# Optimization experiments

Hardware: AMD Instinct MI355X
Metric: run time of the kernel (lower is better)

Reference implementation:

```python
import jax, jax.numpy as jnp
import numpy as np

NU, NI, E, NNZ, NLAYERS, TOPK = 2560, 3584, 64, 200000, 2, 5
N = NU + NI
DQK = 4 * E  # Linear(dim, 4*dim)


def setup_inputs() -> dict:
    key = jax.random.key(0)
    ks = jax.random.split(key, 14)
    s = 1.0 / np.sqrt(E)
    return {
        "user_emb": jax.random.normal(ks[0], (NU, E), jnp.float32) * s,
        "item_emb": jax.random.normal(ks[1], (NI, E), jnp.float32) * s,
        "norm_rows": jax.random.randint(ks[2], (NNZ,), 0, N, jnp.int32),
        "norm_cols": jax.random.randint(ks[3], (NNZ,), 0, N, jnp.int32),
        "norm_vals": jax.random.uniform(ks[4], (NNZ,), jnp.float32) / 32.0,
        "adj_rows": jax.random.randint(ks[5], (NNZ,), 0, N, jnp.int32),
        "adj_cols": jax.random.randint(ks[6], (NNZ,), 0, N, jnp.int32),
        "adj_vals": jnp.ones((NNZ,), jnp.float32),
        "Wq": jax.random.normal(ks[7], (DQK, E), jnp.float32) * s,
        "bq": jnp.zeros((DQK,), jnp.float32),
        "Wk": jax.random.normal(ks[8], (DQK, E), jnp.float32) * s,
        "bk": jnp.zeros((DQK,), jnp.float32),
        "Wv": jax.random.normal(ks[9], (DQK, E), jnp.float32) * s,
        "bv": jnp.zeros((DQK,), jnp.float32),
    }


def reference(user_emb, item_emb, norm_rows, norm_cols, norm_vals,
              adj_rows, adj_cols, adj_vals, Wq, bq, Wk, bk, Wv, bv):
    # densified sparse adjacencies (duplicates accumulated, as COO spmm would)
    A_norm = jnp.zeros((N, N), jnp.float32).at[norm_rows, norm_cols].add(norm_vals)
    A = jnp.zeros((N, N), jnp.float32).at[adj_rows, adj_cols].add(adj_vals)

    ego = jnp.concatenate([user_emb, item_emb], axis=0)  # [N, E]
    layers = []
    att_out = None
    for _ in range(NLAYERS):
        layers.append(ego)
        # GNN propagation: sparse.mm(norm_adj, ego)
        ego = A_norm @ ego  # [N, E]
        # dense similarity + sparse-blended similarity
        sim = ego @ ego.T                      # [N, N]
        sim = sim + 0.5 * (A @ sim)            # [N, N]
        # top-K neighbor selection + gather
        _, idx = jax.lax.top_k(sim, TOPK)      # [N, K]
        sample = ego[idx]                      # [N, K, E]
        # SampleAttention: Linear(dim, 4*dim) Q/K/V, scaled dot-product over K neighbors
        q = ego @ Wq.T + bq                    # [N, 4E]
        kk = sample @ Wk.T + bk                # [N, K, 4E]
        vv = sample @ Wv.T + bv                # [N, K, 4E]
        scores = jnp.einsum('nd,nkd->nk', q, kk) / jnp.sqrt(jnp.float32(DQK))
        att = jax.nn.softmax(scores, axis=-1)
        att_out = jnp.einsum('nk,nkd->nd', att, vv)  # [N, 4E]
    mean_emb = jnp.mean(jnp.stack(layers, axis=1), axis=1)  # [N, E]
    return mean_emb[:NU], mean_emb[NU:], att_out
```

## Files before the change

### kernel.cpp

```cpp
#include <hip/hip_runtime.h>
#include <math.h>

#define NUSER 2560
#define NITEM 3584
#define NN    6144
#define EDIM  64
#define NNZ   200000
#define DQK   256
#define KTOP  5
#define SPLITS 16
#define TPS    3
#define CK     4
#define ELLW   96
#define TPB   256
#define QKV_BLOCKS 576
#define TOPK_BLOCKS (96 * SPLITS)
#define BSTR  72

typedef __attribute__((ext_vector_type(8))) short bf16x8;
typedef __attribute__((ext_vector_type(4))) float f32x4;

__device__ __forceinline__ unsigned short f2bf(float f) {
    unsigned int b = __float_as_uint(f);
    unsigned int r = (b + 0x7FFFu + ((b >> 16) & 1u)) >> 16;
    return (unsigned short)r;
}
__device__ __forceinline__ int pack2(float a, float b) {
    return (int)f2bf(a) | ((int)f2bf(b) << 16);
}
__device__ __forceinline__ void ell_unpack(long long v, int* col, float* w) {
    *col = (int)(v & 0xffffffffLL);
    *w   = __int_as_float((int)(v >> 32));
}
__device__ __forceinline__ unsigned umax(unsigned a, unsigned b) { return a > b ? a : b; }
__device__ __forceinline__ unsigned umin(unsigned a, unsigned b) { return a < b ? a : b; }

__global__ void build_kernel(const int* __restrict__ nr, const int* __restrict__ nc,
                             const float* __restrict__ nv,
                             const int* __restrict__ ar, const int* __restrict__ ac,
                             int* __restrict__ cnt_n, int* __restrict__ cnt_a,
                             long long* __restrict__ cv_n, int* __restrict__ cv_a) {
    int g = blockIdx.x * TPB + threadIdx.x;
    if (g < NNZ) {
        int r = __builtin_nontemporal_load(&nr[g]);
        int c = __builtin_nontemporal_load(&nc[g]);
        float v = __builtin_nontemporal_load(&nv[g]);
        int slot = atomicAdd(&cnt_n[r], 1);
        long long pk = (unsigned int)c | ((long long)(unsigned int)__float_as_int(v) << 32);
        __builtin_nontemporal_store(pk, &cv_n[r * ELLW + slot]);
    } else if (g < 2 * NNZ) {
        int h = g - NNZ;
        int r = __builtin_nontemporal_load(&ar[h]);
        int c = __builtin_nontemporal_load(&ac[h]);
        int slot = atomicAdd(&cnt_a[r], 1);
        __builtin_nontemporal_store(c, &cv_a[r * ELLW + slot]);
    }
}

__global__ __launch_bounds__(TPB) void spmm_ell_emb_kernel(
        const int* __restrict__ cnt, const long long* __restrict__ cv,
        const float* __restrict__ user, const float* __restrict__ item,
        float* __restrict__ dst) {
    int r = blockIdx.x * 4 + (threadIdx.x >> 6);
    int lane = threadIdx.x & 63;
    int s = r * ELLW, e = s + cnt[r];
    float a[8];
#pragma unroll
    for (int u = 0; u < 8; ++u) a[u] = 0.f;
    int j = s, n8 = s + ((e - s) & ~7);
    for (; j < n8; j += 8) {
        int col[8]; float w[8];
#pragma unroll
        for (int u = 0; u < 8; ++u) ell_unpack(__builtin_nontemporal_load(&cv[j + u]), &col[u], &w[u]);
#pragma unroll
        for (int u = 0; u < 8; ++u) {
            float x = (col[u] < NUSER) ? user[col[u] * EDIM + lane]
                                       : item[(col[u] - NUSER) * EDIM + lane];
            a[u] = fmaf(w[u], x, a[u]);
        }
    }
    for (; j < e; ++j) {
        int col; float w;
        ell_unpack(__builtin_nontemporal_load(&cv[j]), &col, &w);
        float x = (col < NUSER) ? user[col * EDIM + lane] : item[(col - NUSER) * EDIM + lane];
        a[0] = fmaf(w, x, a[0]);
    }
    dst[r * EDIM + lane] = ((a[0] + a[1]) + (a[2] + a[3])) + ((a[4] + a[5]) + (a[6] + a[7]));
}

__global__ __launch_bounds__(TPB) void spmm_ell_kernel(
        const int* __restrict__ cnt, const long long* __restrict__ cv,
        const float* __restrict__ src, float* __restrict__ dst,
        unsigned short* __restrict__ dsth) {
    int r = blockIdx.x * 4 + (threadIdx.x >> 6);
    int lane = threadIdx.x & 63;
    int s = r * ELLW, e = s + cnt[r];
    float a[8];
#pragma unroll
    for (int u = 0; u < 8; ++u) a[u] = 0.f;
    int j = s, n8 = s + ((e - s) & ~7);
    for (; j < n8; j += 8) {
        int col[8]; float w[8];
#pragma unroll
        for (int u = 0; u < 8; ++u) ell_unpack(__builtin_nontemporal_load(&cv[j + u]), &col[u], &w[u]);
#pragma unroll
        for (int u = 0; u < 8; ++u)
            a[u] = fmaf(w[u], src[col[u] * EDIM + lane], a[u]);
    }
    for (; j < e; ++j) {
        int col; float w;
        ell_unpack(__builtin_nontemporal_load(&cv[j]), &col, &w);
        a[0] = fmaf(w, src[col * EDIM + lane], a[0]);
    }
    float res = ((a[0] + a[1]) + (a[2] + a[3])) + ((a[4] + a[5]) + (a[6] + a[7]));
    dst[r * EDIM + lane]  = res;
    dsth[r * EDIM + lane] = f2bf(res);
}

__global__ __launch_bounds__(TPB) void qm_mean_kernel(
        const int* __restrict__ cnt, const int* __restrict__ cv,
        const float* __restrict__ ego2, const float* __restrict__ ego1,
        const float* __restrict__ user, const float* __restrict__ item,
        float* __restrict__ Qm, float* __restrict__ outmean) {
    int r = blockIdx.x * 4 + (threadIdx.x >> 6);
    int lane = threadIdx.x & 63;
    int s = r * ELLW, e = s + cnt[r];
    float a[8];
#pragma unroll
    for (int u = 0; u < 8; ++u) a[u] = 0.f;
    int j = s, n8 = s + ((e - s) & ~7);
    for (; j < n8; j += 8) {
        int col[8];
#pragma unroll
        for (int u = 0; u < 8; ++u) col[u] = __builtin_nontemporal_load(&cv[j + u]);
#pragma unroll
        for (int u = 0; u < 8; ++u)
            a[u] += ego2[col[u] * EDIM + lane];
    }
    for (; j < e; ++j) {
        int col = __builtin_nontemporal_load(&cv[j]);
        a[0] += ego2[col * EDIM + lane];
    }
    float acc = ((a[0] + a[1]) + (a[2] + a[3])) + ((a[4] + a[5]) + (a[6] + a[7]));
    int o = r * EDIM + lane;
    Qm[o] = ego2[o] + 0.5f * acc;
    float e0v = (r < NUSER) ? user[o] : item[o - NUSER * EDIM];
    outmean[o] = 0.5f * (e0v + ego1[o]);
}

__global__ __launch_bounds__(TPB) void qkv_gemm_kernel(
        const float* __restrict__ ego2,
        const float* __restrict__ Wq, const float* __restrict__ bq,
        const float* __restrict__ Wk, const float* __restrict__ bk,
        const float* __restrict__ Wv, const float* __restrict__ bv,
        float* __restrict__ Qa, float* __restrict__ Ka, float* __restrict__ Va) {
    __shared__ __align__(16) float smem[12288];
    int t = threadIdx.x;
    int tx = t & 15, ty = t >> 4;
    int id = blockIdx.x;
    int bz = id / 192, rem = id % 192, by = rem / 96, bx = rem % 96;
    const float* W; const float* b; float* out;
    if (bz == 0)      { W = Wq; b = bq; out = Qa; }
    else if (bz == 1) { W = Wk; b = bk; out = Ka; }
    else              { W = Wv; b = bv; out = Va; }
    float* As = smem;
    float* Bs = smem + 4096;
    int r0 = bx * 64, d0 = by * 128;
    {
        int r = t & 63, eb = (t >> 6) * 16;
#pragma unroll
        for (int rep = 0; rep < 4; ++rep) {
            int e0 = eb + rep * 4;
            float4 v = *(const float4*)&ego2[(r0 + r) * EDIM + e0];
            As[(e0 + 0) * 64 + r] = v.x; As[(e0 + 1) * 64 + r] = v.y;
            As[(e0 + 2) * 64 + r] = v.z; As[(e0 + 3) * 64 + r] = v.w;
        }
    }
    {
        int d = t & 127, eb = (t >> 7) * 32;
#pragma unroll
        for (int rep = 0; rep < 8; ++rep) {
            int e0 = eb + rep * 4;
            float4 v = *(const float4*)&W[(d0 + d) * EDIM + e0];
            Bs[(e0 + 0) * 128 + d] = v.x; Bs[(e0 + 1) * 128 + d] = v.y;
            Bs[(e0 + 2) * 128 + d] = v.z; Bs[(e0 + 3) * 128 + d] = v.w;
        }
    }
    __syncthreads();
    float acc[4][8];
#pragma unroll
    for (int i = 0; i < 4; ++i)
#pragma unroll
        for (int j = 0; j < 8; ++j) acc[i][j] = 0.f;
#pragma unroll 4
    for (int e = 0; e < 64; ++e) {
        float4 a  = *(const float4*)&As[e * 64 + ty * 4];
        float4 b0 = *(const float4*)&Bs[e * 128 + tx * 4];
        float4 b1 = *(const float4*)&Bs[e * 128 + 64 + tx * 4];
        float ar[4] = {a.x, a.y, a.z, a.w};
#pragma unroll
        for (int i = 0; i < 4; ++i) {
            acc[i][0] = fmaf(ar[i], b0.x, acc[i][0]);
            acc[i][1] = fmaf(ar[i], b0.y, acc[i][1]);
            acc[i][2] = fmaf(ar[i], b0.z, acc[i][2]);
            acc[i][3] = fmaf(ar[i], b0.w, acc[i][3]);
            acc[i][4] = fmaf(ar[i], b1.x, acc[i][4]);
            acc[i][5] = fmaf(ar[i], b1.y, acc[i][5]);
            acc[i][6] = fmaf(ar[i], b1.z, acc[i][6]);
            acc[i][7] = fmaf(ar[i], b1.w, acc[i][7]);
        }
    }
    float4 bias0 = *(const float4*)&b[d0 + tx * 4];
    float4 bias1 = *(const float4*)&b[d0 + 64 + tx * 4];
#pragma unroll
    for (int i = 0; i < 4; ++i) {
        int r = r0 + ty * 4 + i;
        float4 o0 = make_float4(acc[i][0] + bias0.x, acc[i][1] + bias0.y,
                                acc[i][2] + bias0.z, acc[i][3] + bias0.w);
        float4 o1 = make_float4(acc[i][4] + bias1.x, acc[i][5] + bias1.y,
                                acc[i][6] + bias1.z, acc[i][7] + bias1.w);
        *(float4*)&out[r * DQK + d0 + tx * 4] = o0;
        *(float4*)&out[r * DQK + d0 + 64 + tx * 4] = o1;
    }
}

__global__ __launch_bounds__(TPB) void topk_kernel(
        const unsigned short* __restrict__ eg2h,
        const float* __restrict__ Qm,
        int* __restrict__ pidx) {
    __shared__ __align__(16) short smem[13312];
    int t = threadIdx.x;
    int id = blockIdx.x;
    int rb = id % 96, sp = id / 96;
    int r0 = rb * 64;
    int w = t >> 6, lane = t & 63, lq = lane >> 4, lc = lane & 15;

    short* Ah = smem;
    short* Bh = Ah + 64 * EDIM;

    {
        int row = t >> 2, seg = t & 3;
        const float4* src = (const float4*)&Qm[(size_t)(r0 + row) * EDIM + seg * 16];
        float4 f0 = src[0], f1 = src[1], f2 = src[2], f3 = src[3];
        int4 p0, p1;
        p0.x = pack2(f0.x, f0.y); p0.y = pack2(f0.z, f0.w);
        p0.z = pack2(f1.x, f1.y); p0.w = pack2(f1.z, f1.w);
        p1.x = pack2(f2.x, f2.y); p1.y = pack2(f2.z, f2.w);
        p1.z = pack2(f3.x, f3.y); p1.w = pack2(f3.z, f3.w);
        *(int4*)&Ah[row * EDIM + seg * 16] = p0;
        *(int4*)&Ah[row * EDIM + seg * 16 + 8] = p1;
    }

    int4 pr[4];
    {
        int c0 = (sp * TPS) * 128;
#pragma unroll
        for (int rep = 0; rep < 4; ++rep) {
            int v = t + 256 * rep;
            pr[rep] = *(const int4*)&eg2h[(size_t)(c0 + (v >> 3)) * EDIM + (v & 7) * 8];
        }
    }

    unsigned t3[4][3];
#pragma unroll
    for (int i = 0; i < 4; ++i)
#pragma unroll
        for (int k = 0; k < 3; ++k) t3[i][k] = 0u;

    const unsigned KMASK = 0xFFFFFFC0u;
    bf16x8 af0, af1;
    for (int tile = 0; tile < TPS; ++tile) {
        __syncthreads();
#pragma unroll
        for (int rep = 0; rep < 4; ++rep) {
            int v = t + 256 * rep;
            *(int4*)&Bh[(v >> 3) * BSTR + (v & 7) * 8] = pr[rep];
        }
        if (tile + 1 < TPS) {
            int c1 = (sp * TPS + tile + 1) * 128;
#pragma unroll
            for (int rep = 0; rep < 4; ++rep) {
                int v = t + 256 * rep;
                pr[rep] = *(const int4*)&eg2h[(size_t)(c1 + (v >> 3)) * EDIM + (v & 7) * 8];
            }
        }
        __syncthreads();
        if (tile == 0) {
            af0 = *(const bf16x8*)&Ah[(w * 16 + lc) * EDIM + lq * 8];
            af1 = *(const bf16x8*)&Ah[(w * 16 + lc) * EDIM + 32 + lq * 8];
        }

        int tb = tile * 8;
#pragma unroll
        for (int ch = 0; ch < 8; ++ch) {
            bf16x8 b0 = *(const bf16x8*)&Bh[(ch * 16 + lc) * BSTR + lq * 8];
            bf16x8 b1 = *(const bf16x8*)&Bh[(ch * 16 + lc) * BSTR + 32 + lq * 8];
            f32x4 acc = {16.f, 16.f, 16.f, 16.f};
            acc = __builtin_amdgcn_mfma_f32_16x16x32_bf16(af0, b0, acc, 0, 0, 0);
            acc = __builtin_amdgcn_mfma_f32_16x16x32_bf16(af1, b1, acc, 0, 0, 0);
            unsigned lid = (unsigned)(tb + ch);
#pragma unroll
            for (int reg = 0; reg < 4; ++reg) {
                unsigned key = (__float_as_uint(acc[reg]) & KMASK) | lid;
                unsigned v0 = t3[reg][0], v1 = t3[reg][1], v2 = t3[reg][2];
                t3[reg][0] = umax(v0, key);
                t3[reg][1] = umax(v1, umin(v0, key));
                t3[reg][2] = umax(v2, umin(v1, key));
            }
        }
    }

    int sb128 = sp * (TPS * 128);
    unsigned lc2 = (unsigned)(lc << 2);
#pragma unroll
    for (int i = 0; i < 4; ++i) {
        int row = r0 + w * 16 + lq * 4 + i;
        int base = (row * SPLITS + sp) * CK;
        unsigned a0 = t3[i][0], a1 = t3[i][1], a2 = t3[i][2];
#pragma unroll
        for (int k = 0; k < CK; ++k) {
            unsigned vk = (a0 & KMASK) | lc2;
            unsigned bvv = vk;
#pragma unroll
            for (int off = 1; off < 16; off <<= 1)
                bvv = umax(bvv, (unsigned)__shfl_xor((int)bvv, off, 64));
            if (vk == bvv) {
                unsigned lid = a0 & 63u;
                pidx[base + k] = sb128 + (int)((lid >> 3) << 7) + (int)((lid & 7) << 4) + lc;
                a0 = a1; a1 = a2; a2 = 0u;
            }
        }
    }
}

__global__ __launch_bounds__(TPB) void attn_kernel(
        const float* __restrict__ Qm, const float* __restrict__ ego2,
        const float* __restrict__ Qa, const float* __restrict__ Ka, const float* __restrict__ Va,
        const int* __restrict__ pidx, float* __restrict__ out) {
    __shared__ float sb[4][64];
    int wv = threadIdx.x >> 6, lane = threadIdx.x & 63;
    int r = blockIdx.x * 4 + wv;
    int ci0 = pidx[r * (SPLITS * CK) + lane];
    int part = lane & 3;

    const float4* qmp = (const float4*)(Qm + (size_t)r * EDIM + part * 16);
    float4 q0 = qmp[0], q1 = qmp[1], q2 = qmp[2], q3 = qmp[3];

#pragma unroll
    for (int p = 0; p < 4; ++p) {
        int j = p * 16 + (lane >> 2);
        int c = __shfl(ci0, j, 64);
        const float4* ep = (const float4*)(ego2 + (size_t)c * EDIM + part * 16);
        float4 e0 = ep[0], e1 = ep[1], e2 = ep[2], e3 = ep[3];
        float s = 0.f;
        s = fmaf(q0.x, e0.x, s); s = fmaf(q0.y, e0.y, s); s = fmaf(q0.z, e0.z, s); s = fmaf(q0.w, e0.w, s);
        s = fmaf(q1.x, e1.x, s); s = fmaf(q1.y, e1.y, s); s = fmaf(q1.z, e1.z, s); s = fmaf(q1.w, e1.w, s);
        s = fmaf(q2.x, e2.x, s); s = fmaf(q2.y, e2.y, s); s = fmaf(q2.z, e2.z, s); s = fmaf(q2.w, e2.w, s);
        s = fmaf(q3.x, e3.x, s); s = fmaf(q3.y, e3.y, s); s = fmaf(q3.z, e3.z, s); s = fmaf(q3.w, e3.w, s);
        s += __shfl_xor(s, 1, 64);
        s += __shfl_xor(s, 2, 64);
        if (part == 0) sb[wv][j] = s;
    }
    float sv = sb[wv][lane];

    float prevv = INFINITY; int previ = -1;
    int cI[KTOP];
#pragma unroll
    for (int k = 0; k < KTOP; ++k) {
        bool adm = (sv < prevv) || (sv == prevv && ci0 > previ);
        float bv = adm ? sv : -INFINITY;
        int   bi = adm ? ci0 : 0x7fffffff;
#pragma unroll
        for (int off = 1; off < 64; off <<= 1) {
            float ov = __shfl_xor(bv, off, 64);
            int   oi = __shfl_xor(bi, off, 64);
            if (ov > bv || (ov == bv && oi < bi)) { bv = ov; bi = oi; }
        }
        cI[k] = bi; prevv = bv; previ = bi;
    }

    float4 q = *(const float4*)&Qa[r * DQK + lane * 4];
    float sc[KTOP];
#pragma unroll
    for (int k = 0; k < KTOP; ++k) {
        float4 kk = *(const float4*)&Ka[cI[k] * DQK + lane * 4];
        float p = q.x * kk.x + q.y * kk.y + q.z * kk.z + q.w * kk.w;
#pragma unroll
        for (int off = 32; off; off >>= 1) p += __shfl_xor(p, off, 64);
        sc[k] = p * 0.0625f;
    }
    float m = sc[0];
#pragma unroll
    for (int k = 1; k < KTOP; ++k) m = fmaxf(m, sc[k]);
    float wgt[KTOP], ssum = 0.f;
#pragma unroll
    for (int k = 0; k < KTOP; ++k) { wgt[k] = expf(sc[k] - m); ssum += wgt[k]; }
    float inv = 1.f / ssum;
    float4 o = make_float4(0.f, 0.f, 0.f, 0.f);
#pragma unroll
    for (int k = 0; k < KTOP; ++k) {
        float4 vv = *(const float4*)&Va[cI[k] * DQK + lane * 4];
        float a = wgt[k] * inv;
        o.x = fmaf(a, vv.x, o.x); o.y = fmaf(a, vv.y, o.y);
        o.z = fmaf(a, vv.z, o.z); o.w = fmaf(a, vv.w, o.w);
    }
    *(float4*)&out[r * DQK + lane * 4] = o;
}

extern "C" void kernel_launch(void* const* d_in, const int* in_sizes, int n_in,
                              void* d_out, int out_size, void* d_ws, size_t ws_size,
                              hipStream_t stream) {
    const float* user  = (const float*)d_in[0];
    const float* item  = (const float*)d_in[1];
    const int*   nrows = (const int*)d_in[2];
    const int*   ncols = (const int*)d_in[3];
    const float* nvals = (const float*)d_in[4];
    const int*   arows = (const int*)d_in[5];
    const int*   acols = (const int*)d_in[6];
    const float* Wq = (const float*)d_in[8];  const float* bq = (const float*)d_in[9];
    const float* Wk = (const float*)d_in[10]; const float* bk = (const float*)d_in[11];
    const float* Wv = (const float*)d_in[12]; const float* bv = (const float*)d_in[13];
    float* out = (float*)d_out;
    float* ws  = (float*)d_ws;

    const int NE  = NN * EDIM;
    const int NQK = NN * DQK;
    float* ego1 = ws;
    float* ego2 = ws + NE;
    float* Qm   = ws + 2 * NE;
    float* Qa   = ws + 3 * NE;
    float* Ka   = Qa + NQK;
    float* Va   = Ka + NQK;
    int*   pidx = (int*)(Va + NQK);
    unsigned short* eg2h = (unsigned short*)(pidx + NN * SPLITS * CK);

    int* ell    = (int*)Qa;
    int* cnt_n  = ell;
    int* cnt_a  = ell + 6144;
    long long* cv_n = (long long*)(ell + 12288);
    int* cv_a   = (int*)(cv_n + NN * ELLW);

    hipMemsetAsync(cnt_n, 0, 12288 * sizeof(int), stream);
    build_kernel<<<(2 * NNZ + TPB - 1) / TPB, TPB, 0, stream>>>(nrows, ncols, nvals,
                                                                arows, acols,
                                                                cnt_n, cnt_a, cv_n, cv_a);
    spmm_ell_emb_kernel<<<NN / 4, TPB, 0, stream>>>(cnt_n, cv_n, user, item, ego1);
    spmm_ell_kernel<<<NN / 4, TPB, 0, stream>>>(cnt_n, cv_n, ego1, ego2, eg2h);
    qm_mean_kernel<<<NN / 4, TPB, 0, stream>>>(cnt_a, cv_a, ego2, ego1, user, item, Qm, out);
    topk_kernel<<<TOPK_BLOCKS, TPB, 0, stream>>>(eg2h, Qm, pidx);
    qkv_gemm_kernel<<<QKV_BLOCKS, TPB, 0, stream>>>(ego2, Wq, bq, Wk, bk, Wv, bv, Qa, Ka, Va);
    attn_kernel<<<NN / 4, TPB, 0, stream>>>(Qm, ego2, Qa, Ka, Va, pidx, out + NE);
}
```

Measured before the change: 200.3 us.

## Fuse whole pipeline into one persistent cooperative kernel with grid syncs

Replaces seven kernel launches and a memset with one cooperative persistent kernel that runs each stage in grid-stride loops, separated by grid-wide barriers. The top-k and QKV GEMM stages now share one work loop so they can run concurrently. The GEMM loads its K dimension in two halves so its shared-memory footprint fits inside the top-k buffer. The aim is to remove launch gaps and tail idle time between stages. The cost is grid-sync overhead, a grid capped by occupancy, and register and shared-memory pressure from the merged kernel, which may lower occupancy.

```diff
diff --git a/kernel.cpp b/kernel.cpp
--- a/kernel.cpp
+++ b/kernel.cpp
@@ -1,5 +1,8 @@
 #include <hip/hip_runtime.h>
+#include <hip/hip_cooperative_groups.h>
 #include <math.h>
+
+namespace cg = cooperative_groups;
 
 #define NUSER 2560
 #define NITEM 3584
@@ -35,12 +38,11 @@
 __device__ __forceinline__ unsigned umax(unsigned a, unsigned b) { return a > b ? a : b; }
 __device__ __forceinline__ unsigned umin(unsigned a, unsigned b) { return a < b ? a : b; }
 
-__global__ void build_kernel(const int* __restrict__ nr, const int* __restrict__ nc,
-                             const float* __restrict__ nv,
-                             const int* __restrict__ ar, const int* __restrict__ ac,
-                             int* __restrict__ cnt_n, int* __restrict__ cnt_a,
-                             long long* __restrict__ cv_n, int* __restrict__ cv_a) {
-    int g = blockIdx.x * TPB + threadIdx.x;
+
+__device__ __forceinline__ void build_body(int g,
+        const int* __restrict__ nr, const int* __restrict__ nc, const float* __restrict__ nv,
+        const int* __restrict__ ar, const int* __restrict__ ac,
+        int* cnt_n, int* cnt_a, long long* cv_n, int* cv_a) {
     if (g < NNZ) {
         int r = __builtin_nontemporal_load(&nr[g]);
         int c = __builtin_nontemporal_load(&nc[g]);
@@ -48,7 +50,7 @@
         int slot = atomicAdd(&cnt_n[r], 1);
         long long pk = (unsigned int)c | ((long long)(unsigned int)__float_as_int(v) << 32);
         __builtin_nontemporal_store(pk, &cv_n[r * ELLW + slot]);
-    } else if (g < 2 * NNZ) {
+    } else {
         int h = g - NNZ;
         int r = __builtin_nontemporal_load(&ar[h]);
         int c = __builtin_nontemporal_load(&ac[h]);
@@ -57,12 +59,10 @@
     }
 }
 
-__global__ __launch_bounds__(TPB) void spmm_ell_emb_kernel(
-        const int* __restrict__ cnt, const long long* __restrict__ cv,
+__device__ __forceinline__ void spmm_emb_body(int r, int lane,
+        const int* cnt, const long long* cv,
         const float* __restrict__ user, const float* __restrict__ item,
         float* __restrict__ dst) {
-    int r = blockIdx.x * 4 + (threadIdx.x >> 6);
-    int lane = threadIdx.x & 63;
     int s = r * ELLW, e = s + cnt[r];
     float a[8];
 #pragma unroll
@@ -88,12 +88,10 @@
     dst[r * EDIM + lane] = ((a[0] + a[1]) + (a[2] + a[3])) + ((a[4] + a[5]) + (a[6] + a[7]));
 }
 
-__global__ __launch_bounds__(TPB) void spmm_ell_kernel(
-        const int* __restrict__ cnt, const long long* __restrict__ cv,
+__device__ __forceinline__ void spmm_body(int r, int lane,
+        const int* cnt, const long long* cv,
         const float* __restrict__ src, float* __restrict__ dst,
         unsigned short* __restrict__ dsth) {
-    int r = blockIdx.x * 4 + (threadIdx.x >> 6);
-    int lane = threadIdx.x & 63;
     int s = r * ELLW, e = s + cnt[r];
     float a[8];
 #pragma unroll
@@ -117,13 +115,11 @@
     dsth[r * EDIM + lane] = f2bf(res);
 }
 
-__global__ __launch_bounds__(TPB) void qm_mean_kernel(
-        const int* __restrict__ cnt, const int* __restrict__ cv,
+__device__ __forceinline__ void qm_mean_body(int r, int lane,
+        const int* cnt, const int* cv,
         const float* __restrict__ ego2, const float* __restrict__ ego1,
         const float* __restrict__ user, const float* __restrict__ item,
         float* __restrict__ Qm, float* __restrict__ outmean) {
-    int r = blockIdx.x * 4 + (threadIdx.x >> 6);
-    int lane = threadIdx.x & 63;
     int s = r * ELLW, e = s + cnt[r];
     float a[8];
 #pragma unroll
@@ -148,66 +144,67 @@
     outmean[o] = 0.5f * (e0v + ego1[o]);
 }
 
-__global__ __launch_bounds__(TPB) void qkv_gemm_kernel(
+__device__ __forceinline__ void gemm_body(int id, int t, float* smem,
         const float* __restrict__ ego2,
         const float* __restrict__ Wq, const float* __restrict__ bq,
         const float* __restrict__ Wk, const float* __restrict__ bk,
         const float* __restrict__ Wv, const float* __restrict__ bv,
-        float* __restrict__ Qa, float* __restrict__ Ka, float* __restrict__ Va) {
-    __shared__ __align__(16) float smem[12288];
-    int t = threadIdx.x;
+        float* Qa, float* Ka, float* Va) {
     int tx = t & 15, ty = t >> 4;
-    int id = blockIdx.x;
     int bz = id / 192, rem = id % 192, by = rem / 96, bx = rem % 96;
     const float* W; const float* b; float* out;
     if (bz == 0)      { W = Wq; b = bq; out = Qa; }
     else if (bz == 1) { W = Wk; b = bk; out = Ka; }
     else              { W = Wv; b = bv; out = Va; }
     float* As = smem;
-    float* Bs = smem + 4096;
+    float* Bs = smem + 2048;
     int r0 = bx * 64, d0 = by * 128;
-    {
-        int r = t & 63, eb = (t >> 6) * 16;
-#pragma unroll
-        for (int rep = 0; rep < 4; ++rep) {
-            int e0 = eb + rep * 4;
-            float4 v = *(const float4*)&ego2[(r0 + r) * EDIM + e0];
-            As[(e0 + 0) * 64 + r] = v.x; As[(e0 + 1) * 64 + r] = v.y;
-            As[(e0 + 2) * 64 + r] = v.z; As[(e0 + 3) * 64 + r] = v.w;
-        }
-    }
-    {
-        int d = t & 127, eb = (t >> 7) * 32;
-#pragma unroll
-        for (int rep = 0; rep < 8; ++rep) {
-            int e0 = eb + rep * 4;
-            float4 v = *(const float4*)&W[(d0 + d) * EDIM + e0];
-            Bs[(e0 + 0) * 128 + d] = v.x; Bs[(e0 + 1) * 128 + d] = v.y;
-            Bs[(e0 + 2) * 128 + d] = v.z; Bs[(e0 + 3) * 128 + d] = v.w;
-        }
-    }
-    __syncthreads();
     float acc[4][8];
 #pragma unroll
     for (int i = 0; i < 4; ++i)
 #pragma unroll
         for (int j = 0; j < 8; ++j) acc[i][j] = 0.f;
+
+    for (int h = 0; h < 2; ++h) {
+        if (h) __syncthreads();
+        {
+            int r = t & 63, eb = (t >> 6) * 8;
+#pragma unroll
+            for (int rep = 0; rep < 2; ++rep) {
+                int e0 = eb + rep * 4;
+                float4 v = *(const float4*)&ego2[(r0 + r) * EDIM + h * 32 + e0];
+                As[(e0 + 0) * 64 + r] = v.x; As[(e0 + 1) * 64 + r] = v.y;
+                As[(e0 + 2) * 64 + r] = v.z; As[(e0 + 3) * 64 + r] = v.w;
+            }
+        }
+        {
+            int d = t & 127, eb = (t >> 7) * 16;
+#pragma unroll
+            for (int rep = 0; rep < 4; ++rep) {
+                int e0 = eb + rep * 4;
+                float4 v = *(const float4*)&W[(d0 + d) * EDIM + h * 32 + e0];
+                Bs[(e0 + 0) * 128 + d] = v.x; Bs[(e0 + 1) * 128 + d] = v.y;
+                Bs[(e0 + 2) * 128 + d] = v.z; Bs[(e0 + 3) * 128 + d] = v.w;
+            }
+        }
+        __syncthreads();
 #pragma unroll 4
-    for (int e = 0; e < 64; ++e) {
-        float4 a  = *(const float4*)&As[e * 64 + ty * 4];
-        float4 b0 = *(const float4*)&Bs[e * 128 + tx * 4];
-        float4 b1 = *(const float4*)&Bs[e * 128 + 64 + tx * 4];
-        float ar[4] = {a.x, a.y, a.z, a.w};
-#pragma unroll
-        for (int i = 0; i < 4; ++i) {
-            acc[i][0] = fmaf(ar[i], b0.x, acc[i][0]);
-            acc[i][1] = fmaf(ar[i], b0.y, acc[i][1]);
-            acc[i][2] = fmaf(ar[i], b0.z, acc[i][2]);
-            acc[i][3] = fmaf(ar[i], b0.w, acc[i][3]);
-            acc[i][4] = fmaf(ar[i], b1.x, acc[i][4]);
-            acc[i][5] = fmaf(ar[i], b1.y, acc[i][5]);
-            acc[i][6] = fmaf(ar[i], b1.z, acc[i][6]);
-            acc[i][7] = fmaf(ar[i], b1.w, acc[i][7]);
+        for (int e = 0; e < 32; ++e) {
+            float4 a  = *(const float4*)&As[e * 64 + ty * 4];
+            float4 b0 = *(const float4*)&Bs[e * 128 + tx * 4];
+            float4 b1 = *(const float4*)&Bs[e * 128 + 64 + tx * 4];
+            float ar[4] = {a.x, a.y, a.z, a.w};
+#pragma unroll
+            for (int i = 0; i < 4; ++i) {
+                acc[i][0] = fmaf(ar[i], b0.x, acc[i][0]);
+                acc[i][1] = fmaf(ar[i], b0.y, acc[i][1]);
+                acc[i][2] = fmaf(ar[i], b0.z, acc[i][2]);
+                acc[i][3] = fmaf(ar[i], b0.w, acc[i][3]);
+                acc[i][4] = fmaf(ar[i], b1.x, acc[i][4]);
+                acc[i][5] = fmaf(ar[i], b1.y, acc[i][5]);
+                acc[i][6] = fmaf(ar[i], b1.z, acc[i][6]);
+                acc[i][7] = fmaf(ar[i], b1.w, acc[i][7]);
+            }
         }
     }
     float4 bias0 = *(const float4*)&b[d0 + tx * 4];
@@ -224,13 +221,9 @@
     }
 }
 
-__global__ __launch_bounds__(TPB) void topk_kernel(
+__device__ __forceinline__ void topk_body(int id, int t, short* smem,
         const unsigned short* __restrict__ eg2h,
-        const float* __restrict__ Qm,
-        int* __restrict__ pidx) {
-    __shared__ __align__(16) short smem[13312];
-    int t = threadIdx.x;
-    int id = blockIdx.x;
+        const float* __restrict__ Qm, int* pidx) {
     int rb = id % 96, sp = id / 96;
     int r0 = rb * 64;
     int w = t >> 6, lane = t & 63, lq = lane >> 4, lc = lane & 15;
@@ -333,13 +326,12 @@
     }
 }
 
-__global__ __launch_bounds__(TPB) void attn_kernel(
+__device__ __forceinline__ void attn_body(int u, int t, float (*sb)[64],
         const float* __restrict__ Qm, const float* __restrict__ ego2,
-        const float* __restrict__ Qa, const float* __restrict__ Ka, const float* __restrict__ Va,
+        const float* Qa, const float* Ka, const float* Va,
         const int* __restrict__ pidx, float* __restrict__ out) {
-    __shared__ float sb[4][64];
-    int wv = threadIdx.x >> 6, lane = threadIdx.x & 63;
-    int r = blockIdx.x * 4 + wv;
+    int wv = t >> 6, lane = t & 63;
+    int r = u * 4 + wv;
     int ci0 = pidx[r * (SPLITS * CK) + lane];
     int part = lane & 3;
 
@@ -405,6 +397,98 @@
         o.z = fmaf(a, vv.z, o.z); o.w = fmaf(a, vv.w, o.w);
     }
     *(float4*)&out[r * DQK + lane * 4] = o;
+}
+
+__global__ __launch_bounds__(TPB) void fused_all(
+        const float* __restrict__ user, const float* __restrict__ item,
+        const int* __restrict__ nr, const int* __restrict__ nc, const float* __restrict__ nv,
+        const int* __restrict__ ar, const int* __restrict__ ac,
+        const float* __restrict__ Wq, const float* __restrict__ bq,
+        const float* __restrict__ Wk, const float* __restrict__ bk,
+        const float* __restrict__ Wv, const float* __restrict__ bv,
+        float* __restrict__ ego1, float* __restrict__ ego2, float* __restrict__ Qm,
+        float* Qa, float* Ka, float* Va,
+        int* __restrict__ pidx, unsigned short* __restrict__ eg2h,
+        int* cnt_n, int* cnt_a, long long* cv_n, int* cv_a,
+        float* __restrict__ out) {
+    cg::grid_group grid = cg::this_grid();
+    __shared__ __align__(16) char smem_u[26624];
+    int t = threadIdx.x;
+    int nB = gridDim.x;
+    int wv = t >> 6, lane = t & 63;
+
+    for (int g = blockIdx.x * TPB + t; g < 2 * NN; g += nB * TPB) cnt_n[g] = 0;
+    grid.sync();
+
+    for (int g = blockIdx.x * TPB + t; g < 2 * NNZ; g += nB * TPB)
+        build_body(g, nr, nc, nv, ar, ac, cnt_n, cnt_a, cv_n, cv_a);
+    grid.sync();
+
+    for (int u = blockIdx.x; u < NN / 4; u += nB)
+        spmm_emb_body(u * 4 + wv, lane, cnt_n, cv_n, user, item, ego1);
+    grid.sync();
+
+    for (int u = blockIdx.x; u < NN / 4; u += nB)
+        spmm_body(u * 4 + wv, lane, cnt_n, cv_n, ego1, ego2, eg2h);
+    grid.sync();
+
+    for (int u = blockIdx.x; u < NN / 4; u += nB)
+        qm_mean_body(u * 4 + wv, lane, cnt_a, cv_a, ego2, ego1, user, item, Qm, out);
+    grid.sync();
+
+    for (int u = blockIdx.x; u < TOPK_BLOCKS + QKV_BLOCKS; u += nB) {
+        __syncthreads();
+        if (u < TOPK_BLOCKS)
+            topk_body(u, t, (short*)smem_u, eg2h, Qm, pidx);
+        else
+            gemm_body(u - TOPK_BLOCKS, t, (float*)smem_u, ego2, Wq, bq, Wk, bk, Wv, bv, Qa, Ka, Va);
+    }
+    grid.sync();
+
+    for (int u = blockIdx.x; u < NN / 4; u += nB)
+        attn_body(u, t, (float (*)[64])smem_u, Qm, ego2, Qa, Ka, Va, pidx, out + NN * EDIM);
+}
+
+__global__ void build_kernel(const int* __restrict__ nr, const int* __restrict__ nc,
+                             const float* __restrict__ nv,
+                             const int* __restrict__ ar, const int* __restrict__ ac,
+                             int* cnt_n, int* cnt_a, long long* cv_n, int* cv_a) {
+    int g = blockIdx.x * TPB + threadIdx.x;
+    if (g < 2 * NNZ) build_body(g, nr, nc, nv, ar, ac, cnt_n, cnt_a, cv_n, cv_a);
+}
+__global__ __launch_bounds__(TPB) void spmm_ell_emb_kernel(
+        const int* cnt, const long long* cv,
+        const float* user, const float* item, float* dst) {
+    spmm_emb_body(blockIdx.x * 4 + (threadIdx.x >> 6), threadIdx.x & 63, cnt, cv, user, item, dst);
+}
+__global__ __launch_bounds__(TPB) void spmm_ell_kernel(
+        const int* cnt, const long long* cv,
+        const float* src, float* dst, unsigned short* dsth) {
+    spmm_body(blockIdx.x * 4 + (threadIdx.x >> 6), threadIdx.x & 63, cnt, cv, src, dst, dsth);
+}
+__global__ __launch_bounds__(TPB) void qm_mean_kernel(
+        const int* cnt, const int* cv, const float* ego2, const float* ego1,
+        const float* user, const float* item, float* Qm, float* outmean) {
+    qm_mean_body(blockIdx.x * 4 + (threadIdx.x >> 6), threadIdx.x & 63, cnt, cv, ego2, ego1, user, item, Qm, outmean);
+}
+__global__ __launch_bounds__(TPB) void qkv_gemm_kernel(
+        const float* ego2, const float* Wq, const float* bq,
+        const float* Wk, const float* bk, const float* Wv, const float* bv,
+        float* Qa, float* Ka, float* Va) {
+    __shared__ __align__(16) float smem[6144];
+    gemm_body(blockIdx.x, threadIdx.x, smem, ego2, Wq, bq, Wk, bk, Wv, bv, Qa, Ka, Va);
+}
+__global__ __launch_bounds__(TPB) void topk_kernel(
+        const unsigned short* eg2h, const float* Qm, int* pidx) {
+    __shared__ __align__(16) short smem[13312];
+    topk_body(blockIdx.x, threadIdx.x, smem, eg2h, Qm, pidx);
+}
+__global__ __launch_bounds__(TPB) void attn_kernel(
+        const float* Qm, const float* ego2,
+        const float* Qa, const float* Ka, const float* Va,
+        const int* pidx, float* out) {
+    __shared__ float sb[4][64];
+    attn_body(blockIdx.x, threadIdx.x, sb, Qm, ego2, Qa, Ka, Va, pidx, out);
 }
 
 extern "C" void kernel_launch(void* const* d_in, const int* in_sizes, int n_in,
@@ -440,14 +524,42 @@
     long long* cv_n = (long long*)(ell + 12288);
     int* cv_a   = (int*)(cv_n + NN * ELLW);
 
-    hipMemsetAsync(cnt_n, 0, 12288 * sizeof(int), stream);
-    build_kernel<<<(2 * NNZ + TPB - 1) / TPB, TPB, 0, stream>>>(nrows, ncols, nvals,
-                                                                arows, acols,
-                                                                cnt_n, cnt_a, cv_n, cv_a);
-    spmm_ell_emb_kernel<<<NN / 4, TPB, 0, stream>>>(cnt_n, cv_n, user, item, ego1);
-    spmm_ell_kernel<<<NN / 4, TPB, 0, stream>>>(cnt_n, cv_n, ego1, ego2, eg2h);
-    qm_mean_kernel<<<NN / 4, TPB, 0, stream>>>(cnt_a, cv_a, ego2, ego1, user, item, Qm, out);
-    topk_kernel<<<TOPK_BLOCKS, TPB, 0, stream>>>(eg2h, Qm, pidx);
-    qkv_gemm_kernel<<<QKV_BLOCKS, TPB, 0, stream>>>(ego2, Wq, bq, Wk, bk, Wv, bv, Qa, Ka, Va);
-    attn_kernel<<<NN / 4, TPB, 0, stream>>>(Qm, ego2, Qa, Ka, Va, pidx, out + NE);
-}
+    static int G = 0;
+    if (G == 0) {
+        int maxb = 0;
+        hipError_t e1 = hipOccupancyMaxActiveBlocksPerMultiprocessor(&maxb, fused_all, TPB, 0);
+        int ncu = 256;
+        hipDeviceProp_t prop;
+        if (hipGetDeviceProperties(&prop, 0) == hipSuccess && prop.multiProcessorCount > 0)
+            ncu = prop.multiProcessorCount;
+        if (e1 != hipSuccess || maxb < 1) maxb = 3;
+        long g = (long)maxb * (long)ncu;
+        G = (g > TOPK_BLOCKS) ? TOPK_BLOCKS : (int)g;
+        if (G < 64) G = 64;
+    }
+
+    void* args[] = {
+        (void*)&user, (void*)&item,
+        (void*)&nrows, (void*)&ncols, (void*)&nvals,
+        (void*)&arows, (void*)&acols,
+        (void*)&Wq, (void*)&bq, (void*)&Wk, (void*)&bk, (void*)&Wv, (void*)&bv,
+        (void*)&ego1, (void*)&ego2, (void*)&Qm,
+        (void*)&Qa, (void*)&Ka, (void*)&Va,
+        (void*)&pidx, (void*)&eg2h,
+        (void*)&cnt_n, (void*)&cnt_a, (void*)&cv_n, (void*)&cv_a,
+        (void*)&out };
+
+    hipError_t err = hipLaunchCooperativeKernel(fused_all, dim3(G), dim3(TPB), args, 0, stream);
+    if (err != hipSuccess) {
+        hipMemsetAsync(cnt_n, 0, 12288 * sizeof(int), stream);
+        build_kernel<<<(2 * NNZ + TPB - 1) / TPB, TPB, 0, stream>>>(nrows, ncols, nvals,
+                                                                    arows, acols,
+                                                                    cnt_n, cnt_a, cv_n, cv_a);
+        spmm_ell_emb_kernel<<<NN / 4, TPB, 0, stream>>>(cnt_n, cv_n, user, item, ego1);
+        spmm_ell_kernel<<<NN / 4, TPB, 0, stream>>>(cnt_n, cv_n, ego1, ego2, eg2h);
+        qm_mean_kernel<<<NN / 4, TPB, 0, stream>>>(cnt_a, cv_a, ego2, ego1, user, item, Qm, out);
+        topk_kernel<<<TOPK_BLOCKS, TPB, 0, stream>>>(eg2h, Qm, pidx);
+        qkv_gemm_kernel<<<QKV_BLOCKS, TPB, 0, stream>>>(ego2, Wq, bq, Wk, bk, Wv, bv, Qa, Ka, Va);
+        attn_kernel<<<NN / 4, TPB, 0, stream>>>(Qm, ego2, Qa, Ka, Va, pidx, out + NE);
+    }
+}
```

Measured after the change: 493.0 us. +146.2%, slower.

## Merge top-k and QKV GEMM into one launch and use grid-stride persistent blocks

Applied to the files above, without the earlier changes.

Turns each kernel body into a device function and launches the kernels with fixed grid sizes that loop over work units, so fewer blocks are launched. The top-k and QKV GEMM stages now run in one kernel: the first 768 blocks each handle two top-k units and the remaining blocks run the GEMM tiles, so the two independent stages can overlap on the GPU. This cuts one launch and should improve CU fill. The risk is load imbalance, since top-k blocks do twice as much work while GEMM blocks do one tile. Shared memory is now sized for the larger of the two stages.

```diff
diff --git a/kernel.cpp b/kernel.cpp
--- a/kernel.cpp
+++ b/kernel.cpp
@@ -13,9 +13,13 @@
 #define CK     4
 #define ELLW   96
 #define TPB   256
-#define QKV_BLOCKS 576
-#define TOPK_BLOCKS (96 * SPLITS)
 #define BSTR  72
+
+#define BUILD_BLOCKS 512
+#define UNIT_BLOCKS  768
+#define TOPK_UNITS   (96 * SPLITS)
+#define TOPK_BLOCKS  768
+#define GEMM_UNITS   576
 
 typedef __attribute__((ext_vector_type(8))) short bf16x8;
 typedef __attribute__((ext_vector_type(4))) float f32x4;
@@ -35,34 +39,11 @@
 __device__ __forceinline__ unsigned umax(unsigned a, unsigned b) { return a > b ? a : b; }
 __device__ __forceinline__ unsigned umin(unsigned a, unsigned b) { return a < b ? a : b; }
 
-__global__ void build_kernel(const int* __restrict__ nr, const int* __restrict__ nc,
-                             const float* __restrict__ nv,
-                             const int* __restrict__ ar, const int* __restrict__ ac,
-                             int* __restrict__ cnt_n, int* __restrict__ cnt_a,
-                             long long* __restrict__ cv_n, int* __restrict__ cv_a) {
-    int g = blockIdx.x * TPB + threadIdx.x;
-    if (g < NNZ) {
-        int r = __builtin_nontemporal_load(&nr[g]);
-        int c = __builtin_nontemporal_load(&nc[g]);
-        float v = __builtin_nontemporal_load(&nv[g]);
-        int slot = atomicAdd(&cnt_n[r], 1);
-        long long pk = (unsigned int)c | ((long long)(unsigned int)__float_as_int(v) << 32);
-        __builtin_nontemporal_store(pk, &cv_n[r * ELLW + slot]);
-    } else if (g < 2 * NNZ) {
-        int h = g - NNZ;
-        int r = __builtin_nontemporal_load(&ar[h]);
-        int c = __builtin_nontemporal_load(&ac[h]);
-        int slot = atomicAdd(&cnt_a[r], 1);
-        __builtin_nontemporal_store(c, &cv_a[r * ELLW + slot]);
-    }
-}
-
-__global__ __launch_bounds__(TPB) void spmm_ell_emb_kernel(
-        const int* __restrict__ cnt, const long long* __restrict__ cv,
+
+__device__ __forceinline__ void spmm_emb_body(int r, int lane,
+        const int* cnt, const long long* cv,
         const float* __restrict__ user, const float* __restrict__ item,
         float* __restrict__ dst) {
-    int r = blockIdx.x * 4 + (threadIdx.x >> 6);
-    int lane = threadIdx.x & 63;
     int s = r * ELLW, e = s + cnt[r];
     float a[8];
 #pragma unroll
@@ -88,12 +69,10 @@
     dst[r * EDIM + lane] = ((a[0] + a[1]) + (a[2] + a[3])) + ((a[4] + a[5]) + (a[6] + a[7]));
 }
 
-__global__ __launch_bounds__(TPB) void spmm_ell_kernel(
-        const int* __restrict__ cnt, const long long* __restrict__ cv,
+__device__ __forceinline__ void spmm_body(int r, int lane,
+        const int* cnt, const long long* cv,
         const float* __restrict__ src, float* __restrict__ dst,
         unsigned short* __restrict__ dsth) {
-    int r = blockIdx.x * 4 + (threadIdx.x >> 6);
-    int lane = threadIdx.x & 63;
     int s = r * ELLW, e = s + cnt[r];
     float a[8];
 #pragma unroll
@@ -117,13 +96,11 @@
     dsth[r * EDIM + lane] = f2bf(res);
 }
 
-__global__ __launch_bounds__(TPB) void qm_mean_kernel(
-        const int* __restrict__ cnt, const int* __restrict__ cv,
+__device__ __forceinline__ void qm_mean_body(int r, int lane,
+        const int* cnt, const int* cv,
         const float* __restrict__ ego2, const float* __restrict__ ego1,
         const float* __restrict__ user, const float* __restrict__ item,
         float* __restrict__ Qm, float* __restrict__ outmean) {
-    int r = blockIdx.x * 4 + (threadIdx.x >> 6);
-    int lane = threadIdx.x & 63;
     int s = r * ELLW, e = s + cnt[r];
     float a[8];
 #pragma unroll
@@ -148,16 +125,13 @@
     outmean[o] = 0.5f * (e0v + ego1[o]);
 }
 
-__global__ __launch_bounds__(TPB) void qkv_gemm_kernel(
+__device__ __forceinline__ void gemm_body(int id, int t, float* smem,
         const float* __restrict__ ego2,
         const float* __restrict__ Wq, const float* __restrict__ bq,
         const float* __restrict__ Wk, const float* __restrict__ bk,
         const float* __restrict__ Wv, const float* __restrict__ bv,
-        float* __restrict__ Qa, float* __restrict__ Ka, float* __restrict__ Va) {
-    __shared__ __align__(16) float smem[12288];
-    int t = threadIdx.x;
+        float* Qa, float* Ka, float* Va) {
     int tx = t & 15, ty = t >> 4;
-    int id = blockIdx.x;
     int bz = id / 192, rem = id % 192, by = rem / 96, bx = rem % 96;
     const float* W; const float* b; float* out;
     if (bz == 0)      { W = Wq; b = bq; out = Qa; }
@@ -224,13 +198,9 @@
     }
 }
 
-__global__ __launch_bounds__(TPB) void topk_kernel(
+__device__ __forceinline__ void topk_body(int id, int t, short* smem,
         const unsigned short* __restrict__ eg2h,
-        const float* __restrict__ Qm,
-        int* __restrict__ pidx) {
-    __shared__ __align__(16) short smem[13312];
-    int t = threadIdx.x;
-    int id = blockIdx.x;
+        const float* __restrict__ Qm, int* pidx) {
     int rb = id % 96, sp = id / 96;
     int r0 = rb * 64;
     int w = t >> 6, lane = t & 63, lq = lane >> 4, lc = lane & 15;
@@ -333,13 +303,12 @@
     }
 }
 
-__global__ __launch_bounds__(TPB) void attn_kernel(
+__device__ __forceinline__ void attn_body(int u, int t, float (*sb)[64],
         const float* __restrict__ Qm, const float* __restrict__ ego2,
-        const float* __restrict__ Qa, const float* __restrict__ Ka, const float* __restrict__ Va,
+        const float* Qa, const float* Ka, const float* Va,
         const int* __restrict__ pidx, float* __restrict__ out) {
-    __shared__ float sb[4][64];
-    int wv = threadIdx.x >> 6, lane = threadIdx.x & 63;
-    int r = blockIdx.x * 4 + wv;
+    int wv = t >> 6, lane = t & 63;
+    int r = u * 4 + wv;
     int ci0 = pidx[r * (SPLITS * CK) + lane];
     int part = lane & 3;
 
@@ -405,6 +374,79 @@
         o.z = fmaf(a, vv.z, o.z); o.w = fmaf(a, vv.w, o.w);
     }
     *(float4*)&out[r * DQK + lane * 4] = o;
+}
+
+
+__global__ void build_kernel(const int* __restrict__ nr, const int* __restrict__ nc,
+                             const float* __restrict__ nv,
+                             const int* __restrict__ ar, const int* __restrict__ ac,
+                             int* cnt_n, int* cnt_a, long long* cv_n, int* cv_a) {
+    for (int g = blockIdx.x * TPB + threadIdx.x; g < 2 * NNZ; g += BUILD_BLOCKS * TPB) {
+        if (g < NNZ) {
+            int r = __builtin_nontemporal_load(&nr[g]);
+            int c = __builtin_nontemporal_load(&nc[g]);
+            float v = __builtin_nontemporal_load(&nv[g]);
+            int slot = atomicAdd(&cnt_n[r], 1);
+            long long pk = (unsigned int)c | ((long long)(unsigned int)__float_as_int(v) << 32);
+            __builtin_nontemporal_store(pk, &cv_n[r * ELLW + slot]);
+        } else {
+            int h = g - NNZ;
+            int r = __builtin_nontemporal_load(&ar[h]);
+            int c = __builtin_nontemporal_load(&ac[h]);
+            int slot = atomicAdd(&cnt_a[r], 1);
+            __builtin_nontemporal_store(c, &cv_a[r * ELLW + slot]);
+        }
+    }
+}
+
+__global__ __launch_bounds__(TPB) void spmm_ell_emb_kernel(
+        const int* cnt, const long long* cv,
+        const float* user, const float* item, float* dst) {
+    int wv = threadIdx.x >> 6, lane = threadIdx.x & 63;
+    for (int u = blockIdx.x; u < NN / 4; u += UNIT_BLOCKS)
+        spmm_emb_body(u * 4 + wv, lane, cnt, cv, user, item, dst);
+}
+
+__global__ __launch_bounds__(TPB) void spmm_ell_kernel(
+        const int* cnt, const long long* cv,
+        const float* src, float* dst, unsigned short* dsth) {
+    int wv = threadIdx.x >> 6, lane = threadIdx.x & 63;
+    for (int u = blockIdx.x; u < NN / 4; u += UNIT_BLOCKS)
+        spmm_body(u * 4 + wv, lane, cnt, cv, src, dst, dsth);
+}
+
+__global__ __launch_bounds__(TPB) void qm_mean_kernel(
+        const int* cnt, const int* cv, const float* ego2, const float* ego1,
+        const float* user, const float* item, float* Qm, float* outmean) {
+    int wv = threadIdx.x >> 6, lane = threadIdx.x & 63;
+    for (int u = blockIdx.x; u < NN / 4; u += UNIT_BLOCKS)
+        qm_mean_body(u * 4 + wv, lane, cnt, cv, ego2, ego1, user, item, Qm, outmean);
+}
+
+__global__ __launch_bounds__(TPB) void topk_gemm_kernel(
+        const unsigned short* eg2h, const float* Qm, int* pidx,
+        const float* ego2,
+        const float* Wq, const float* bq, const float* Wk, const float* bk,
+        const float* Wv, const float* bv,
+        float* Qa, float* Ka, float* Va) {
+    __shared__ __align__(16) float smem[12288];
+    int bid = blockIdx.x, t = threadIdx.x;
+    if (bid < TOPK_BLOCKS) {
+        topk_body(bid, t, (short*)smem, eg2h, Qm, pidx);
+        __syncthreads();
+        topk_body(bid + TOPK_BLOCKS, t, (short*)smem, eg2h, Qm, pidx);
+    } else {
+        gemm_body(bid - TOPK_BLOCKS, t, smem, ego2, Wq, bq, Wk, bk, Wv, bv, Qa, Ka, Va);
+    }
+}
+
+__global__ __launch_bounds__(TPB) void attn_kernel(
+        const float* Qm, const float* ego2,
+        const float* Qa, const float* Ka, const float* Va,
+        const int* pidx, float* out) {
+    __shared__ float sb[4][64];
+    for (int u = blockIdx.x; u < NN / 4; u += UNIT_BLOCKS)
+        attn_body(u, threadIdx.x, sb, Qm, ego2, Qa, Ka, Va, pidx, out);
 }
 
 extern "C" void kernel_launch(void* const* d_in, const int* in_sizes, int n_in,
@@ -441,13 +483,12 @@
     int* cv_a   = (int*)(cv_n + NN * ELLW);
 
     hipMemsetAsync(cnt_n, 0, 12288 * sizeof(int), stream);
-    build_kernel<<<(2 * NNZ + TPB - 1) / TPB, TPB, 0, stream>>>(nrows, ncols, nvals,
-                                                                arows, acols,
-                                                                cnt_n, cnt_a, cv_n, cv_a);
-    spmm_ell_emb_kernel<<<NN / 4, TPB, 0, stream>>>(cnt_n, cv_n, user, item, ego1);
-    spmm_ell_kernel<<<NN / 4, TPB, 0, stream>>>(cnt_n, cv_n, ego1, ego2, eg2h);
-    qm_mean_kernel<<<NN / 4, TPB, 0, stream>>>(cnt_a, cv_a, ego2, ego1, user, item, Qm, out);
-    topk_kernel<<<TOPK_BLOCKS, TPB, 0, stream>>>(eg2h, Qm, pidx);
-    qkv_gemm_kernel<<<QKV_BLOCKS, TPB, 0, stream>>>(ego2, Wq, bq, Wk, bk, Wv, bv, Qa, Ka, Va);
-    attn_kernel<<<NN / 4, TPB, 0, stream>>>(Qm, ego2, Qa, Ka, Va, pidx, out + NE);
-}
+    build_kernel<<<BUILD_BLOCKS, TPB, 0, stream>>>(nrows, ncols, nvals, arows, acols,
+                                                   cnt_n, cnt_a, cv_n, cv_a);
+    spmm_ell_emb_kernel<<<UNIT_BLOCKS, TPB, 0, stream>>>(cnt_n, cv_n, user, item, ego1);
+    spmm_ell_kernel<<<UNIT_BLOCKS, TPB, 0, stream>>>(cnt_n, cv_n, ego1, ego2, eg2h);
+    qm_mean_kernel<<<UNIT_BLOCKS, TPB, 0, stream>>>(cnt_a, cv_a, ego2, ego1, user, item, Qm, out);
+    topk_gemm_kernel<<<TOPK_BLOCKS + GEMM_UNITS, TPB, 0, stream>>>(
+        eg2h, Qm, pidx, ego2, Wq, bq, Wk, bk, Wv, bv, Qa, Ka, Va);
+    attn_kernel<<<UNIT_BLOCKS, TPB, 0, stream>>>(Qm, ego2, Qa, Ka, Va, pidx, out + NE);
+}
```

New measurement: 215.9 us. 1.08x slower.
